# Kernel tuning notes

Measured on AMD Instinct MI355X. Metric: run time of the kernel, lower is better.

## Reference

```python
import jax, jax.numpy as jnp
import numpy as np

G, L, NSTA, NSRC, K = 10000, 1000, 400, 2000, 15
SIG = 10.0
FTRNS_SCALE = 1000.0  # ftrns1_diff(x) = x * 1000 (km -> m style linear transform)
FUDGE = 1.0


def setup_inputs() -> dict:
    key = jax.random.key(0)
    ks = jax.random.split(key, 9)
    sta = 10.0 * jax.random.normal(ks[0], (NSTA, 3), jnp.float32)
    src = 10.0 * jax.random.normal(ks[1], (NSRC, 3), jnp.float32)
    mag = jax.random.normal(ks[2], (NSRC,), jnp.float32)
    phase = jax.random.randint(ks[3], (NSTA,), 0, 2)
    x_grid = 10.0 * jax.random.normal(ks[4], (G, 3), jnp.float32)
    locs_ref = 10.0 * jax.random.normal(ks[5], (L, 3), jnp.float32)
    mag_coef = jnp.ones(2, jnp.float32)
    epicenter_spatial_coef = jnp.ones(2, jnp.float32)
    depth_spatial_coef = 0.1 * jax.random.normal(ks[6], (2,), jnp.float32)
    coefs = 0.1 * jax.random.normal(ks[7], (G, L, 2), jnp.float32)
    coefs_ker = SIG + 0.1 * jax.random.normal(ks[8], (G, L, 3), jnp.float32)
    return {"sta": sta, "src": src, "mag": mag, "phase": phase,
            "x_grid": x_grid, "locs_ref": locs_ref, "mag_coef": mag_coef,
            "epicenter_spatial_coef": epicenter_spatial_coef,
            "depth_spatial_coef": depth_spatial_coef,
            "coefs": coefs, "coefs_ker": coefs_ker}


def _ftrns(x):
    return x * FTRNS_SCALE


def _magnitude_fwd(sta, src, mag, phase, x_grid, locs_ref, mag_coef,
                   epicenter_spatial_coef, depth_spatial_coef, coefs, coefs_ker):
    sp = jax.nn.softplus
    zvec = jnp.array([1.0, 1.0, 0.0], dtype=sta.dtype)

    # nearest reference station index for each station (knn k=1)
    locs_ref_cart = _ftrns(locs_ref) / 1000.0            # [L,3]
    sta_pos = _ftrns(sta) / 1000.0                       # [Nsta,3]
    d2_ref = ((sta_pos[:, None, :] - locs_ref_cart[None, :, :]) ** 2).sum(-1)
    sta_ind = jnp.argmin(d2_ref, axis=1)                 # [Nsta]

    # pairwise log-distance matrices [Nsrc, Nsta]
    pw_log_dist_zero = jnp.log10(
        jnp.linalg.norm(_ftrns(src * zvec)[:, None, :] - _ftrns(sta * zvec)[None, :, :], axis=2) + FUDGE)
    pw_log_dist_depths = jnp.log10(jnp.abs(src[:, 2][:, None] - sta[:, 2][None, :]) + FUDGE)

    # --- anisotropic kNN interpolation of coefs[:, sta_ind, :] from grid to src ---
    pos1 = _ftrns(x_grid) / 1000.0                       # [G,3]
    pos2 = _ftrns(src) / 1000.0                          # [Nsrc,3]
    dq = ((pos2[:, None, :] - pos1[None, :, :]) ** 2).sum(-1)  # [Nsrc,G]
    _, idx = jax.lax.top_k(-dq, K)                       # [Nsrc,K] nearest grid nodes

    coefs_sub = coefs[:, sta_ind, :]                     # [G,Nsta,2]
    ker_sub = coefs_ker[:, sta_ind, :]                   # [G,Nsta,3]

    diff = pos1[idx] - pos2[:, None, :]                  # [Nsrc,K,3]
    ker_e = sp(ker_sub[idx])                             # [Nsrc,K,Nsta,3]
    w = jnp.exp(-0.5 * ((diff[:, :, None, :] / ker_e) ** 2).sum(-1))  # [Nsrc,K,Nsta]
    wsum = w.sum(axis=1, keepdims=True)                  # [Nsrc,1,Nsta]
    wsum = jnp.where(wsum == 0.0, 1.0, wsum)
    w = w / wsum
    bias_l = jnp.einsum('qkn,qknc->qnc', w, coefs_sub[idx])  # [Nsrc,Nsta,2]

    # phase-selected bias and coefficients
    bias = jnp.where(phase[None, :] == 0, bias_l[:, :, 0], bias_l[:, :, 1])  # [Nsrc,Nsta]
    mc = sp(mag_coef)[phase]                             # [Nsta]
    ec = sp(epicenter_spatial_coef)[phase]
    dc = depth_spatial_coef[phase]

    log_amp = (mag[:, None] * mc[None, :]
               - ec[None, :] * pw_log_dist_zero
               + dc[None, :] * pw_log_dist_depths
               + bias)                                   # [Nsrc,Nsta]
    return log_amp


def reference(sta, src, mag, phase, x_grid, locs_ref, mag_coef,
              epicenter_spatial_coef, depth_spatial_coef, coefs, coefs_ker):
    return _magnitude_fwd(sta, src, mag, phase, x_grid, locs_ref, mag_coef,
                          epicenter_spatial_coef, depth_spatial_coef, coefs, coefs_ker)
```

## Files before the change

### kernel.cpp

```cpp
#include <hip/hip_runtime.h>
#include <hip/hip_fp16.h>
#include <cstddef>

#define G_N   10000
#define L_N   1000
#define NSTA  400
#define NSRC  2000
#define KK    15
#define CAP   2048
#define LDSB  20480
#define CTLO  (1024 + 8 * CAP)

__device__ __forceinline__ float tr1k(float x) {
    return (x * 1000.0f) / 1000.0f;
}

__device__ __forceinline__ float softplus(float x) {
    return fmaxf(x, 0.0f) + log1pf(expf(-fabsf(x)));
}

__device__ __forceinline__ float softplus_fast(float x) {
    return fmaxf(x, 0.0f) + __logf(1.0f + __expf(-fabsf(x)));
}

__device__ __forceinline__ bool lexless(float v1, int i1, float v2, int i2) {
    return (v1 < v2) || (v1 == v2 && i1 < i2);
}

__global__ void sta_prep_kernel(const float* __restrict__ sta,
                                const float* __restrict__ locs_ref,
                                const float* __restrict__ x_grid,
                                const float* __restrict__ src,
                                int* __restrict__ sta_ind,
                                float* __restrict__ tg,
                                float* __restrict__ ts) {
#pragma clang fp contract(off)
    const int i    = blockIdx.x;
    const int lane = threadIdx.x;

    const int z = i * 64 + lane;
    for (int p = z; p < 3 * (G_N + NSRC); p += 400 * 64) {
        if (p < 3 * G_N) tg[p] = tr1k(x_grid[p]);
        else             ts[p - 3 * G_N] = tr1k(src[p - 3 * G_N]);
    }

    const float sx = tr1k(sta[i * 3 + 0]);
    const float sy = tr1k(sta[i * 3 + 1]);
    const float sz = tr1k(sta[i * 3 + 2]);
    float best = INFINITY;
    int   bidx = 0x7fffffff;
    for (int j = lane; j < L_N; j += 64) {
        float dx = sx - tr1k(locs_ref[j * 3 + 0]);
        float dy = sy - tr1k(locs_ref[j * 3 + 1]);
        float dz = sz - tr1k(locs_ref[j * 3 + 2]);
        float d  = (dx * dx + dy * dy) + dz * dz;
        if (lexless(d, j, best, bidx)) { best = d; bidx = j; }
    }
    for (int off = 1; off < 64; off <<= 1) {
        float ov = __shfl_xor(best, off);
        int   oi = __shfl_xor(bidx, off);
        if (lexless(ov, oi, best, bidx)) { best = ov; bidx = oi; }
    }
    if (lane == 0) sta_ind[i] = bidx;
}

__device__ __forceinline__ void topk_block(int s,
                                           const float* __restrict__ tg,
                                           const float* __restrict__ ts,
                                           int* __restrict__ idx_out,
                                           char* s_raw, int tid) {
#pragma clang fp contract(off)
    const int lane = tid & 63;
    const int wv   = tid >> 6;

    float* s_min  = (float*)s_raw;
    int*   s_cand = (int*)(s_raw + 1024);
    float* s_cd   = (float*)(s_raw + 1024 + 4 * CAP);
    float* s_T    = (float*)(s_raw + CTLO);
    int*   s_cnt  = (int*)(s_raw + CTLO + 4);
    float* s_mv   = (float*)(s_raw + CTLO + 8);
    int*   s_mi   = (int*)(s_raw + CTLO + 24);
    int*   s_ch   = (int*)(s_raw + CTLO + 40);

    if (tid == 0) *s_cnt = 0;

    const float sx = ts[s * 3 + 0];
    const float sy = ts[s * 3 + 1];
    const float sz = ts[s * 3 + 2];

    float mymin = INFINITY;
    for (int g = tid; g < G_N; g += 256) {
        float dx = sx - tg[g * 3 + 0];
        float dy = sy - tg[g * 3 + 1];
        float dz = sz - tg[g * 3 + 2];
        float d  = (dx * dx + dy * dy) + dz * dz;
        mymin = fminf(mymin, d);
    }
    s_min[tid] = mymin;
    __syncthreads();

    if (wv == 0) {
        float m0 = s_min[lane];
        float m1 = s_min[lane + 64];
        float m2 = s_min[lane + 128];
        float m3 = s_min[lane + 192];
        float T = INFINITY;
        for (int r = 0; r < KK; ++r) {
            float lv = m0; int ls = 0;
            if (m1 < lv) { lv = m1; ls = 1; }
            if (m2 < lv) { lv = m2; ls = 2; }
            if (m3 < lv) { lv = m3; ls = 3; }
            float v = lv; int wl = lane;
            for (int off = 1; off < 64; off <<= 1) {
                float ov = __shfl_xor(v, off);
                int   ol = __shfl_xor(wl, off);
                if (ov < v || (ov == v && ol < wl)) { v = ov; wl = ol; }
            }
            T = v;
            if (wl == lane) {
                if (ls == 0) m0 = INFINITY;
                else if (ls == 1) m1 = INFINITY;
                else if (ls == 2) m2 = INFINITY;
                else m3 = INFINITY;
            }
        }
        if (lane == 0) *s_T = T;
    }
    __syncthreads();
    const float T = *s_T;

    for (int g = tid; g < G_N; g += 256) {
        float dx = sx - tg[g * 3 + 0];
        float dy = sy - tg[g * 3 + 1];
        float dz = sz - tg[g * 3 + 2];
        float d  = (dx * dx + dy * dy) + dz * dz;
        if (d <= T) {
            int p = atomicAdd(s_cnt, 1);
            if (p < CAP) { s_cand[p] = g; s_cd[p] = d; }
        }
    }
    __syncthreads();
    const int n = *s_cnt;

    if (n <= CAP) {
        if (wv == 0) {
            float vals[KK];
            int   ids[KK];
#pragma unroll
            for (int j = 0; j < KK; ++j) { vals[j] = INFINITY; ids[j] = 0x7fffffff; }
            for (int c = lane; c < n; c += 64) {
                int   g = s_cand[c];
                float d = s_cd[c];
                if (lexless(d, g, vals[KK - 1], ids[KK - 1])) {
                    float cv = d; int ci = g;
#pragma unroll
                    for (int j = 0; j < KK; ++j) {
                        bool sw = lexless(cv, ci, vals[j], ids[j]);
                        float tv = sw ? vals[j] : cv;
                        int   ti = sw ? ids[j]  : ci;
                        vals[j]  = sw ? cv : vals[j];
                        ids[j]   = sw ? ci : ids[j];
                        cv = tv; ci = ti;
                    }
                }
            }
            for (int r = 0; r < KK; ++r) {
                float v  = vals[0];
                int   id = ids[0];
                int   who = lane;
                for (int off = 1; off < 64; off <<= 1) {
                    float ov = __shfl_xor(v, off);
                    int   oi = __shfl_xor(id, off);
                    int   ow = __shfl_xor(who, off);
                    if (lexless(ov, oi, v, id)) { v = ov; id = oi; who = ow; }
                }
                if (lane == 0) idx_out[s * KK + r] = id;
                if (who == lane) {
#pragma unroll
                    for (int j = 0; j < KK - 1; ++j) { vals[j] = vals[j + 1]; ids[j] = ids[j + 1]; }
                    vals[KK - 1] = INFINITY;
                    ids[KK - 1]  = 0x7fffffff;
                }
            }
        }
    } else {
        for (int r = 0; r < KK; ++r) {
            float v  = INFINITY;
            int   id = 0x7fffffff;
            for (int g = tid; g < G_N; g += 256) {
                bool skip = false;
                for (int j = 0; j < r; ++j) skip = skip || (s_ch[j] == g);
                if (skip) continue;
                float dx = sx - tg[g * 3 + 0];
                float dy = sy - tg[g * 3 + 1];
                float dz = sz - tg[g * 3 + 2];
                float d  = (dx * dx + dy * dy) + dz * dz;
                if (lexless(d, g, v, id)) { v = d; id = g; }
            }
            for (int off = 1; off < 64; off <<= 1) {
                float ov = __shfl_xor(v, off);
                int   oi = __shfl_xor(id, off);
                if (lexless(ov, oi, v, id)) { v = ov; id = oi; }
            }
            if (lane == 0) { s_mv[wv] = v; s_mi[wv] = id; }
            __syncthreads();
            if (tid == 0) {
                float bv = s_mv[0]; int bi = s_mi[0];
                for (int w = 1; w < 4; ++w)
                    if (lexless(s_mv[w], s_mi[w], bv, bi)) { bv = s_mv[w]; bi = s_mi[w]; }
                s_ch[r] = bi;
                idx_out[s * KK + r] = bi;
            }
            __syncthreads();
        }
    }
}

__device__ __forceinline__ void pack_block(int g,
                                           const float* __restrict__ coefs,
                                           const float* __restrict__ coefs_ker,
                                           const int* __restrict__ sta_ind,
                                           const int* __restrict__ phase,
                                           uint2* __restrict__ pk,
                                           char* s_raw, int tid) {
    float* s_ker = (float*)s_raw;
    float* s_c   = (float*)(s_raw + 12288);

    const float4* kr4 = (const float4*)(coefs_ker + (size_t)g * (L_N * 3));
    const float4* cr4 = (const float4*)(coefs     + (size_t)g * (L_N * 2));
    float4* sk4 = (float4*)s_ker;
    float4* sc4 = (float4*)s_c;
#pragma unroll
    for (int j = 0; j < 3; ++j) {
        int p = tid + j * 256;
        if (p < (L_N * 3) / 4) sk4[p] = kr4[p];
    }
#pragma unroll
    for (int j = 0; j < 2; ++j) {
        int p = tid + j * 256;
        if (p < (L_N * 2) / 4) sc4[p] = cr4[p];
    }
    const int i1  = tid + 256;
    const int st0 = sta_ind[tid];
    const int ph0 = phase[tid];
    const int st1 = (i1 < NSTA) ? sta_ind[i1] : 0;
    const int ph1 = (i1 < NSTA) ? phase[i1] : 0;
    __syncthreads();

    {
        float rk0 = 1.0f / softplus_fast(s_ker[st0 * 3 + 0]);
        float rk1 = 1.0f / softplus_fast(s_ker[st0 * 3 + 1]);
        float rk2 = 1.0f / softplus_fast(s_ker[st0 * 3 + 2]);
        float c   = (ph0 == 0) ? s_c[st0 * 2 + 0] : s_c[st0 * 2 + 1];
        __half2 a = __floats2half2_rn(rk0, rk1);
        __half2 b = __floats2half2_rn(rk2, c);
        uint2 u;
        u.x = *reinterpret_cast<unsigned int*>(&a);
        u.y = *reinterpret_cast<unsigned int*>(&b);
        pk[(size_t)g * NSTA + tid] = u;
    }
    if (i1 < NSTA) {
        float rk0 = 1.0f / softplus_fast(s_ker[st1 * 3 + 0]);
        float rk1 = 1.0f / softplus_fast(s_ker[st1 * 3 + 1]);
        float rk2 = 1.0f / softplus_fast(s_ker[st1 * 3 + 2]);
        float c   = (ph1 == 0) ? s_c[st1 * 2 + 0] : s_c[st1 * 2 + 1];
        __half2 a = __floats2half2_rn(rk0, rk1);
        __half2 b = __floats2half2_rn(rk2, c);
        uint2 u;
        u.x = *reinterpret_cast<unsigned int*>(&a);
        u.y = *reinterpret_cast<unsigned int*>(&b);
        pk[(size_t)g * NSTA + i1] = u;
    }
}

__global__ __launch_bounds__(256, 8) void fused_kernel(
    const float* __restrict__ coefs, const float* __restrict__ coefs_ker,
    const int* __restrict__ sta_ind, const int* __restrict__ phase,
    uint2* __restrict__ pk,
    const float* __restrict__ tg, const float* __restrict__ ts,
    int* __restrict__ idx_out)
{
    __shared__ __align__(16) char s_raw[LDSB];
    const int bid = blockIdx.x;
    const int t = bid / 6, r = bid % 6;
    if (r == 5) {
        topk_block(t, tg, ts, idx_out, s_raw, threadIdx.x);
    } else {
        pack_block(t * 5 + r, coefs, coefs_ker, sta_ind, phase, pk, s_raw, threadIdx.x);
    }
}

__global__ __launch_bounds__(256, 8) void topk_only_kernel(
    const float* __restrict__ tg, const float* __restrict__ ts,
    int* __restrict__ idx_out)
{
    __shared__ __align__(16) char s_raw[LDSB];
    topk_block(blockIdx.x, tg, ts, idx_out, s_raw, threadIdx.x);
}

__global__ __launch_bounds__(256) void magnitude_fast_kernel(
    const float* __restrict__ sta, const float* __restrict__ src,
    const float* __restrict__ mag, const int* __restrict__ phase,
    const float* __restrict__ x_grid,
    const float* __restrict__ mag_coef, const float* __restrict__ epi_coef,
    const float* __restrict__ dep_coef,
    const uint2* __restrict__ pk, const int* __restrict__ idx,
    float* __restrict__ out)
{
    const int s   = blockIdx.x;
    const int tid = threadIdx.x;

    __shared__ float s_diff[KK][3];
    __shared__ int   s_g[KK];

    if (tid < KK) {
        int g = idx[s * KK + tid];
        s_g[tid] = g;
        s_diff[tid][0] = tr1k(x_grid[g * 3 + 0]) - tr1k(src[s * 3 + 0]);
        s_diff[tid][1] = tr1k(x_grid[g * 3 + 1]) - tr1k(src[s * 3 + 1]);
        s_diff[tid][2] = tr1k(x_grid[g * 3 + 2]) - tr1k(src[s * 3 + 2]);
    }
    __syncthreads();

    const float mag_s = mag[s];
    const float srcx = src[s * 3 + 0];
    const float srcy = src[s * 3 + 1];
    const float srcz = src[s * 3 + 2];
    const float sp_mc0 = softplus(mag_coef[0]), sp_mc1 = softplus(mag_coef[1]);
    const float sp_ec0 = softplus(epi_coef[0]), sp_ec1 = softplus(epi_coef[1]);
    const float dc0 = dep_coef[0], dc1 = dep_coef[1];

    for (int i = tid; i < NSTA; i += 256) {
        float wsum = 0.0f, a = 0.0f;
#pragma unroll
        for (int k = 0; k < KK; ++k) {
            uint2 u = pk[(size_t)s_g[k] * NSTA + i];
            __half2 h01 = *reinterpret_cast<const __half2*>(&u.x);
            __half2 h23 = *reinterpret_cast<const __half2*>(&u.y);
            float2 f01 = __half22float2(h01);
            float2 f23 = __half22float2(h23);
            float t0 = s_diff[k][0] * f01.x;
            float t1 = s_diff[k][1] * f01.y;
            float t2 = s_diff[k][2] * f23.x;
            float e  = __expf(-0.5f * ((t0 * t0 + t1 * t1) + t2 * t2));
            wsum += e;
            a    += e * f23.y;
        }
        if (wsum == 0.0f) wsum = 1.0f;

        const int ph = phase[i];
        float bias = a / wsum;

        float dx = srcx * 1000.0f - sta[i * 3 + 0] * 1000.0f;
        float dy = srcy * 1000.0f - sta[i * 3 + 1] * 1000.0f;
        float lz = __log10f(__fsqrt_rn(dx * dx + dy * dy) + 1.0f);
        float ld = __log10f(fabsf(srcz - sta[i * 3 + 2]) + 1.0f);

        float mc = (ph == 0) ? sp_mc0 : sp_mc1;
        float ec = (ph == 0) ? sp_ec0 : sp_ec1;
        float dc = (ph == 0) ? dc0 : dc1;

        out[(size_t)s * NSTA + i] = mag_s * mc - ec * lz + dc * ld + bias;
    }
}

__global__ __launch_bounds__(256) void magnitude_kernel(
    const float* __restrict__ sta, const float* __restrict__ src,
    const float* __restrict__ mag, const int* __restrict__ phase,
    const float* __restrict__ x_grid,
    const float* __restrict__ mag_coef, const float* __restrict__ epi_coef,
    const float* __restrict__ dep_coef,
    const float* __restrict__ coefs, const float* __restrict__ coefs_ker,
    const int* __restrict__ sta_ind, const int* __restrict__ idx,
    float* __restrict__ out)
{
    const int s   = blockIdx.x;
    const int tid = threadIdx.x;

    __shared__ float s_diff[KK][3];
    __shared__ int   s_g[KK];
    __shared__ int   s_sta[NSTA];

    if (tid < KK) {
        int g = idx[s * KK + tid];
        s_g[tid] = g;
        s_diff[tid][0] = tr1k(x_grid[g * 3 + 0]) - tr1k(src[s * 3 + 0]);
        s_diff[tid][1] = tr1k(x_grid[g * 3 + 1]) - tr1k(src[s * 3 + 1]);
        s_diff[tid][2] = tr1k(x_grid[g * 3 + 2]) - tr1k(src[s * 3 + 2]);
    }
    for (int i = tid; i < NSTA; i += 256) s_sta[i] = sta_ind[i];
    __syncthreads();

    const float mag_s = mag[s];
    const float srcx = src[s * 3 + 0];
    const float srcy = src[s * 3 + 1];
    const float srcz = src[s * 3 + 2];
    const float sp_mc0 = softplus(mag_coef[0]), sp_mc1 = softplus(mag_coef[1]);
    const float sp_ec0 = softplus(epi_coef[0]), sp_ec1 = softplus(epi_coef[1]);
    const float dc0 = dep_coef[0], dc1 = dep_coef[1];

    for (int i = tid; i < NSTA; i += 256) {
        const int st = s_sta[i];
        float wsum = 0.0f, a0 = 0.0f, a1 = 0.0f;
#pragma unroll
        for (int k = 0; k < KK; ++k) {
            const int g = s_g[k];
            const float* kp = coefs_ker + ((size_t)g * L_N + st) * 3;
            float k0 = softplus(kp[0]);
            float k1 = softplus(kp[1]);
            float k2 = softplus(kp[2]);
            float t0 = s_diff[k][0] / k0;
            float t1 = s_diff[k][1] / k1;
            float t2 = s_diff[k][2] / k2;
            float e  = expf(-0.5f * ((t0 * t0 + t1 * t1) + t2 * t2));
            const float* cp = coefs + ((size_t)g * L_N + st) * 2;
            wsum += e;
            a0 += e * cp[0];
            a1 += e * cp[1];
        }
        if (wsum == 0.0f) wsum = 1.0f;

        const int ph = phase[i];
        float bias = ((ph == 0) ? a0 : a1) / wsum;

        float dx = srcx * 1000.0f - sta[i * 3 + 0] * 1000.0f;
        float dy = srcy * 1000.0f - sta[i * 3 + 1] * 1000.0f;
        float lz = log10f(sqrtf(dx * dx + dy * dy) + 1.0f);
        float ld = log10f(fabsf(srcz - sta[i * 3 + 2]) + 1.0f);

        float mc = (ph == 0) ? sp_mc0 : sp_mc1;
        float ec = (ph == 0) ? sp_ec0 : sp_ec1;
        float dc = (ph == 0) ? dc0 : dc1;

        out[(size_t)s * NSTA + i] = mag_s * mc - ec * lz + dc * ld + bias;
    }
}

extern "C" void kernel_launch(void* const* d_in, const int* in_sizes, int n_in,
                              void* d_out, int out_size, void* d_ws, size_t ws_size,
                              hipStream_t stream) {
    const float* sta       = (const float*)d_in[0];
    const float* src       = (const float*)d_in[1];
    const float* mag       = (const float*)d_in[2];
    const int*   phase     = (const int*)d_in[3];
    const float* x_grid    = (const float*)d_in[4];
    const float* locs_ref  = (const float*)d_in[5];
    const float* mag_coef  = (const float*)d_in[6];
    const float* epi_coef  = (const float*)d_in[7];
    const float* dep_coef  = (const float*)d_in[8];
    const float* coefs     = (const float*)d_in[9];
    const float* coefs_ker = (const float*)d_in[10];
    float* out = (float*)d_out;

    const size_t pk_bytes = (size_t)G_N * NSTA * sizeof(uint2);
    const size_t tail_ints = (size_t)NSRC * KK + NSTA + 3 * G_N + 3 * NSRC;
    const size_t need_fast = pk_bytes + tail_ints * 4;

    if (ws_size >= need_fast) {
        uint2* ws_pk   = (uint2*)d_ws;
        int*   ws_idx  = (int*)((char*)d_ws + pk_bytes);
        int*   ws_sta  = ws_idx + (size_t)NSRC * KK;
        float* ws_tg   = (float*)(ws_sta + NSTA);
        float* ws_ts   = ws_tg + 3 * G_N;

        hipLaunchKernelGGL(sta_prep_kernel, dim3(NSTA), dim3(64), 0, stream,
                           sta, locs_ref, x_grid, src, ws_sta, ws_tg, ws_ts);
        hipLaunchKernelGGL(fused_kernel, dim3(6 * NSRC), dim3(256), 0, stream,
                           coefs, coefs_ker, ws_sta, phase, ws_pk,
                           ws_tg, ws_ts, ws_idx);
        hipLaunchKernelGGL(magnitude_fast_kernel, dim3(NSRC), dim3(256), 0, stream,
                           sta, src, mag, phase, x_grid,
                           mag_coef, epi_coef, dep_coef,
                           ws_pk, ws_idx, out);
    } else {
        int*   ws_sta = (int*)d_ws;
        int*   ws_idx = ws_sta + NSTA;
        float* ws_tg  = (float*)(ws_idx + (size_t)NSRC * KK);
        float* ws_ts  = ws_tg + 3 * G_N;

        hipLaunchKernelGGL(sta_prep_kernel, dim3(NSTA), dim3(64), 0, stream,
                           sta, locs_ref, x_grid, src, ws_sta, ws_tg, ws_ts);
        hipLaunchKernelGGL(topk_only_kernel, dim3(NSRC), dim3(256), 0, stream,
                           ws_tg, ws_ts, ws_idx);
        hipLaunchKernelGGL(magnitude_kernel, dim3(NSRC), dim3(256), 0, stream,
                           sta, src, mag, phase, x_grid,
                           mag_coef, epi_coef, dep_coef,
                           coefs, coefs_ker, ws_sta, ws_idx, out);
    }
}
```

Measured before the change: 136.6 us.

## Pack only grid rows selected by kNN, splitting fused kernel into topk then pack

The fused kernel, which interleaved top-k blocks with packing every grid row's coefs and coefs_ker, is split into a top-k kernel that marks the grid points it selects in a 'used' flag array, followed by a pack kernel that returns early for unmarked grid rows. This avoids reading and packing the large coefs and coefs_ker rows for grid points no source uses. In exchange it serializes top-k before packing, losing the overlap the fused launch gave, and adds a flag buffer and its reset. The candidate capacity CAP also drops from 2048 to 512, which makes the slow fallback path more likely when many candidates tie at the threshold.

```diff
diff --git a/kernel.cpp b/kernel.cpp
--- a/kernel.cpp
+++ b/kernel.cpp
@@ -7,9 +7,7 @@
 #define NSTA  400
 #define NSRC  2000
 #define KK    15
-#define CAP   2048
-#define LDSB  20480
-#define CTLO  (1024 + 8 * CAP)
+#define CAP   512
 
 __device__ __forceinline__ float tr1k(float x) {
     return (x * 1000.0f) / 1000.0f;
@@ -33,7 +31,8 @@
                                 const float* __restrict__ src,
                                 int* __restrict__ sta_ind,
                                 float* __restrict__ tg,
-                                float* __restrict__ ts) {
+                                float* __restrict__ ts,
+                                int* __restrict__ used) {
 #pragma clang fp contract(off)
     const int i    = blockIdx.x;
     const int lane = threadIdx.x;
@@ -43,6 +42,7 @@
         if (p < 3 * G_N) tg[p] = tr1k(x_grid[p]);
         else             ts[p - 3 * G_N] = tr1k(src[p - 3 * G_N]);
     }
+    if (used && z < G_N) used[z] = 0;
 
     const float sx = tr1k(sta[i * 3 + 0]);
     const float sy = tr1k(sta[i * 3 + 1]);
@@ -64,25 +64,26 @@
     if (lane == 0) sta_ind[i] = bidx;
 }
 
-__device__ __forceinline__ void topk_block(int s,
-                                           const float* __restrict__ tg,
-                                           const float* __restrict__ ts,
-                                           int* __restrict__ idx_out,
-                                           char* s_raw, int tid) {
+__global__ __launch_bounds__(256, 8) void topk_only_kernel(
+    const float* __restrict__ tg, const float* __restrict__ ts,
+    int* __restrict__ idx_out, int* __restrict__ used)
+{
 #pragma clang fp contract(off)
+    const int s    = blockIdx.x;
+    const int tid  = threadIdx.x;
     const int lane = tid & 63;
     const int wv   = tid >> 6;
 
-    float* s_min  = (float*)s_raw;
-    int*   s_cand = (int*)(s_raw + 1024);
-    float* s_cd   = (float*)(s_raw + 1024 + 4 * CAP);
-    float* s_T    = (float*)(s_raw + CTLO);
-    int*   s_cnt  = (int*)(s_raw + CTLO + 4);
-    float* s_mv   = (float*)(s_raw + CTLO + 8);
-    int*   s_mi   = (int*)(s_raw + CTLO + 24);
-    int*   s_ch   = (int*)(s_raw + CTLO + 40);
-
-    if (tid == 0) *s_cnt = 0;
+    __shared__ float s_min[256];
+    __shared__ int   s_cand[CAP];
+    __shared__ float s_cd[CAP];
+    __shared__ float s_T;
+    __shared__ int   s_cnt;
+    __shared__ float s_mv[4];
+    __shared__ int   s_mi[4];
+    __shared__ int   s_ch[KK];
+
+    if (tid == 0) s_cnt = 0;
 
     const float sx = ts[s * 3 + 0];
     const float sy = ts[s * 3 + 1];
@@ -124,10 +125,10 @@
                 else m3 = INFINITY;
             }
         }
-        if (lane == 0) *s_T = T;
-    }
-    __syncthreads();
-    const float T = *s_T;
+        if (lane == 0) s_T = T;
+    }
+    __syncthreads();
+    const float T = s_T;
 
     for (int g = tid; g < G_N; g += 256) {
         float dx = sx - tg[g * 3 + 0];
@@ -135,12 +136,12 @@
         float dz = sz - tg[g * 3 + 2];
         float d  = (dx * dx + dy * dy) + dz * dz;
         if (d <= T) {
-            int p = atomicAdd(s_cnt, 1);
+            int p = atomicAdd(&s_cnt, 1);
             if (p < CAP) { s_cand[p] = g; s_cd[p] = d; }
         }
     }
     __syncthreads();
-    const int n = *s_cnt;
+    const int n = s_cnt;
 
     if (n <= CAP) {
         if (wv == 0) {
@@ -174,7 +175,10 @@
                     int   ow = __shfl_xor(who, off);
                     if (lexless(ov, oi, v, id)) { v = ov; id = oi; who = ow; }
                 }
-                if (lane == 0) idx_out[s * KK + r] = id;
+                if (lane == 0) {
+                    idx_out[s * KK + r] = id;
+                    if (used) used[id] = 1;
+                }
                 if (who == lane) {
 #pragma unroll
                     for (int j = 0; j < KK - 1; ++j) { vals[j] = vals[j + 1]; ids[j] = ids[j + 1]; }
@@ -210,21 +214,25 @@
                     if (lexless(s_mv[w], s_mi[w], bv, bi)) { bv = s_mv[w]; bi = s_mi[w]; }
                 s_ch[r] = bi;
                 idx_out[s * KK + r] = bi;
+                if (used) used[bi] = 1;
             }
             __syncthreads();
         }
     }
 }
 
-__device__ __forceinline__ void pack_block(int g,
-                                           const float* __restrict__ coefs,
-                                           const float* __restrict__ coefs_ker,
-                                           const int* __restrict__ sta_ind,
-                                           const int* __restrict__ phase,
-                                           uint2* __restrict__ pk,
-                                           char* s_raw, int tid) {
-    float* s_ker = (float*)s_raw;
-    float* s_c   = (float*)(s_raw + 12288);
+__global__ __launch_bounds__(256, 8) void pack_kernel(
+    const float* __restrict__ coefs, const float* __restrict__ coefs_ker,
+    const int* __restrict__ sta_ind, const int* __restrict__ phase,
+    const int* __restrict__ used,
+    uint2* __restrict__ pk)
+{
+    const int g = blockIdx.x;
+    if (!used[g]) return;
+    const int tid = threadIdx.x;
+
+    __shared__ float s_ker[L_N * 3];
+    __shared__ float s_c[L_N * 2];
 
     const float4* kr4 = (const float4*)(coefs_ker + (size_t)g * (L_N * 3));
     const float4* cr4 = (const float4*)(coefs     + (size_t)g * (L_N * 2));
@@ -273,32 +281,7 @@
     }
 }
 
-__global__ __launch_bounds__(256, 8) void fused_kernel(
-    const float* __restrict__ coefs, const float* __restrict__ coefs_ker,
-    const int* __restrict__ sta_ind, const int* __restrict__ phase,
-    uint2* __restrict__ pk,
-    const float* __restrict__ tg, const float* __restrict__ ts,
-    int* __restrict__ idx_out)
-{
-    __shared__ __align__(16) char s_raw[LDSB];
-    const int bid = blockIdx.x;
-    const int t = bid / 6, r = bid % 6;
-    if (r == 5) {
-        topk_block(t, tg, ts, idx_out, s_raw, threadIdx.x);
-    } else {
-        pack_block(t * 5 + r, coefs, coefs_ker, sta_ind, phase, pk, s_raw, threadIdx.x);
-    }
-}
-
-__global__ __launch_bounds__(256, 8) void topk_only_kernel(
-    const float* __restrict__ tg, const float* __restrict__ ts,
-    int* __restrict__ idx_out)
-{
-    __shared__ __align__(16) char s_raw[LDSB];
-    topk_block(blockIdx.x, tg, ts, idx_out, s_raw, threadIdx.x);
-}
-
-__global__ __launch_bounds__(256) void magnitude_fast_kernel(
+__global__ __launch_bounds__(256, 8) void magnitude_fast_kernel(
     const float* __restrict__ sta, const float* __restrict__ src,
     const float* __restrict__ mag, const int* __restrict__ phase,
     const float* __restrict__ x_grid,
@@ -453,35 +436,37 @@
     float* out = (float*)d_out;
 
     const size_t pk_bytes = (size_t)G_N * NSTA * sizeof(uint2);
-    const size_t tail_ints = (size_t)NSRC * KK + NSTA + 3 * G_N + 3 * NSRC;
+    const size_t tail_ints = (size_t)NSRC * KK + NSTA + G_N + 3 * G_N + 3 * NSRC;
     const size_t need_fast = pk_bytes + tail_ints * 4;
 
     if (ws_size >= need_fast) {
         uint2* ws_pk   = (uint2*)d_ws;
         int*   ws_idx  = (int*)((char*)d_ws + pk_bytes);
         int*   ws_sta  = ws_idx + (size_t)NSRC * KK;
-        float* ws_tg   = (float*)(ws_sta + NSTA);
+        int*   ws_used = ws_sta + NSTA;
+        float* ws_tg   = (float*)(ws_used + G_N);
         float* ws_ts   = ws_tg + 3 * G_N;
 
         hipLaunchKernelGGL(sta_prep_kernel, dim3(NSTA), dim3(64), 0, stream,
-                           sta, locs_ref, x_grid, src, ws_sta, ws_tg, ws_ts);
-        hipLaunchKernelGGL(fused_kernel, dim3(6 * NSRC), dim3(256), 0, stream,
-                           coefs, coefs_ker, ws_sta, phase, ws_pk,
-                           ws_tg, ws_ts, ws_idx);
+                           sta, locs_ref, x_grid, src, ws_sta, ws_tg, ws_ts, ws_used);
+        hipLaunchKernelGGL(topk_only_kernel, dim3(NSRC), dim3(256), 0, stream,
+                           ws_tg, ws_ts, ws_idx, ws_used);
+        hipLaunchKernelGGL(pack_kernel, dim3(G_N), dim3(256), 0, stream,
+                           coefs, coefs_ker, ws_sta, phase, ws_used, ws_pk);
         hipLaunchKernelGGL(magnitude_fast_kernel, dim3(NSRC), dim3(256), 0, stream,
                            sta, src, mag, phase, x_grid,
                            mag_coef, epi_coef, dep_coef,
                            ws_pk, ws_idx, out);
     } else {
-        int*   ws_sta = (int*)d_ws;
-        int*   ws_idx = ws_sta + NSTA;
-        float* ws_tg  = (float*)(ws_idx + (size_t)NSRC * KK);
-        float* ws_ts  = ws_tg + 3 * G_N;
+        int*   ws_sta  = (int*)d_ws;
+        int*   ws_idx  = ws_sta + NSTA;
+        float* ws_tg   = (float*)(ws_idx + (size_t)NSRC * KK);
+        float* ws_ts   = ws_tg + 3 * G_N;
 
         hipLaunchKernelGGL(sta_prep_kernel, dim3(NSTA), dim3(64), 0, stream,
-                           sta, locs_ref, x_grid, src, ws_sta, ws_tg, ws_ts);
+                           sta, locs_ref, x_grid, src, ws_sta, ws_tg, ws_ts, (int*)nullptr);
         hipLaunchKernelGGL(topk_only_kernel, dim3(NSRC), dim3(256), 0, stream,
-                           ws_tg, ws_ts, ws_idx);
+                           ws_tg, ws_ts, ws_idx, (int*)nullptr);
         hipLaunchKernelGGL(magnitude_kernel, dim3(NSRC), dim3(256), 0, stream,
                            sta, src, mag, phase, x_grid,
                            mag_coef, epi_coef, dep_coef,
```

Result: faster. 122.0 us (-10.7%).
